# Performance work log

Hardware: AMD Instinct MI355X
Metric: run time of the kernel (lower is better)

The kernel has to match this reference:

```python
import jax, jax.numpy as jnp
import numpy as np


def _lin_relu(V, W, b):
    # LinearEmbedding: matmul + bias + ReLU (with_act_func=True default)
    return jax.nn.relu(jnp.matmul(V, W) + b)


def setup_inputs() -> dict:
    key = jax.random.key(0)
    ks = jax.random.split(key, 8)
    B, N, F = 4, 4096, 512
    C = F // 8
    sx = 1.0 / np.sqrt(F)
    return {
        "V": jax.random.normal(ks[0], (B, N, F), dtype=jnp.float32),
        "Wf": jax.random.normal(ks[1], (F, C), dtype=jnp.float32) * sx,
        "bf": jax.random.normal(ks[2], (C,), dtype=jnp.float32) * 5e-5 + 1e-4,
        "Wg": jax.random.normal(ks[3], (F, C), dtype=jnp.float32) * sx,
        "bg": jax.random.normal(ks[4], (C,), dtype=jnp.float32) * 5e-5 + 1e-4,
        "Wh": jax.random.normal(ks[5], (F, F), dtype=jnp.float32) * sx,
        "bh": jax.random.normal(ks[6], (F,), dtype=jnp.float32) * 5e-5 + 1e-4,
        "gamma": jax.random.normal(ks[7], (F,), dtype=jnp.float32),
    }


def reference(V, Wf, bf, Wg, bg, Wh, bh, gamma):
    f_out = _lin_relu(V, Wf, bf)          # [B, N, C]
    g_out = _lin_relu(V, Wg, bg)          # [B, N, C]
    h_out = _lin_relu(V, Wh, bh)          # [B, N, F]
    scores = jnp.einsum('bnc,bmc->bnm', f_out, g_out)  # [B, N, N]
    s = jax.nn.softmax(scores, axis=-1)
    o = jnp.einsum('bnm,bmf->bnf', s, h_out)            # [B, N, F]
    return gamma * o + V
```

## Files before the change

### kernel.cpp

```cpp
#include <hip/hip_runtime.h>
#include <hip/hip_bf16.h>
#include <math.h>

#define M_ROWS 16384
#define F_DIM 512
#define C_DIM 64

typedef short bf16x8 __attribute__((ext_vector_type(8)));
typedef float floatx4 __attribute__((ext_vector_type(4)));
typedef unsigned short ushortx8 __attribute__((ext_vector_type(8)));
typedef unsigned short ushortx4 __attribute__((ext_vector_type(4)));

static __device__ __forceinline__ unsigned short f2bf(float x) {
    __hip_bfloat16 h = __float2bfloat16(x);
    return *reinterpret_cast<unsigned short*>(&h);
}
static __device__ __forceinline__ float bf2f(unsigned short h) {
    unsigned int u = ((unsigned int)h) << 16;
    return __builtin_bit_cast(float, u);
}

static __device__ __forceinline__ void lgkm_barrier() {
    asm volatile("s_waitcnt lgkmcnt(0)\n\ts_barrier" ::: "memory");
}


__global__ __launch_bounds__(64) void prep_w_kernel(
    const float* __restrict__ Wf, const float* __restrict__ Wg,
    const float* __restrict__ Wh,
    unsigned short* __restrict__ wt_hi, unsigned short* __restrict__ wt_lo)
{
    const int c = blockIdx.x;
    const int t = threadIdx.x;
    const float* W; int ld, cl;
    if (c < 64)       { W = Wf; ld = C_DIM; cl = c; }
    else if (c < 128) { W = Wg; ld = C_DIM; cl = c - 64; }
    else              { W = Wh; ld = F_DIM; cl = c - 128; }
    const int ng = c >> 4, l16 = c & 15;
    for (int k = t; k < F_DIM; k += 64) {
        const float x = W[(size_t)k * ld + cl];
        const unsigned short h = f2bf(x);
        const int kh = k >> 5, qd = (k >> 3) & 3, j = k & 7;
        const size_t off = (((size_t)(ng * 16 + kh) * 64) + qd * 16 + l16) * 8 + j;
        wt_hi[off] = h;
        wt_lo[off] = f2bf(x - bf2f(h));
    }
}

#define BM 64
#define LDK 72

__global__ __launch_bounds__(256, 4) void embed_mfma_kernel(
    const float* __restrict__ V,
    const unsigned short* __restrict__ wt_hi, const unsigned short* __restrict__ wt_lo,
    const float* __restrict__ bf, const float* __restrict__ bg,
    const float* __restrict__ bh,
    unsigned short* __restrict__ f_bf, unsigned short* __restrict__ g_bf,
    unsigned short* __restrict__ h_sw)
{
    __shared__ __align__(16) unsigned short a_hi[BM][LDK];
    __shared__ __align__(16) unsigned short a_lo[BM][LDK];

    const int t  = threadIdx.x;
    const int R0 = blockIdx.x * BM;
    const bool fg = (blockIdx.y == 0);
    const int cbase = fg ? 0 : blockIdx.y * 128;

    const int w = t >> 6, lane = t & 63, quad = lane >> 4, l16 = lane & 15;

    floatx4 acc[4][2];
    #pragma unroll
    for (int rt = 0; rt < 4; ++rt)
        #pragma unroll
        for (int c = 0; c < 2; ++c)
            acc[rt][c] = (floatx4){0.f, 0.f, 0.f, 0.f};

    const int arow = t >> 4;
    const int acol = (t & 15) * 4;
    const int ng0  = (cbase >> 4) + w * 2;

    #pragma unroll 1
    for (int k0 = 0; k0 < F_DIM; k0 += 64) {
        lgkm_barrier();
        #pragma unroll
        for (int rr = 0; rr < 4; ++rr) {
            const int row = rr * 16 + arow;
            const float4 x = *(const float4*)(V + (size_t)(R0 + row) * F_DIM + k0 + acol);
            const float xs[4] = {x.x, x.y, x.z, x.w};
            ushortx4 hi, lo;
            #pragma unroll
            for (int jj = 0; jj < 4; ++jj) {
                const unsigned short hb2 = f2bf(xs[jj]);
                hi[jj] = hb2;
                lo[jj] = f2bf(xs[jj] - bf2f(hb2));
            }
            *(ushortx4*)&a_hi[row][acol] = hi;
            if (fg) *(ushortx4*)&a_lo[row][acol] = lo;
        }
        lgkm_barrier();
        #pragma unroll
        for (int kk = 0; kk < 2; ++kk) {
            const int kh = (k0 >> 5) + kk;
            const bf16x8 b0 = *(const bf16x8*)(wt_hi + (((size_t)(ng0 * 16 + kh)) * 64 + lane) * 8);
            const bf16x8 b1 = *(const bf16x8*)(wt_hi + (((size_t)((ng0 + 1) * 16 + kh)) * 64 + lane) * 8);
            bf16x8 ah[4];
            #pragma unroll
            for (int rt = 0; rt < 4; ++rt)
                ah[rt] = *(const bf16x8*)&a_hi[rt * 16 + l16][kk * 32 + quad * 8];
            #pragma unroll
            for (int rt = 0; rt < 4; ++rt) {
                acc[rt][0] = __builtin_amdgcn_mfma_f32_16x16x32_bf16(ah[rt], b0, acc[rt][0], 0, 0, 0);
                acc[rt][1] = __builtin_amdgcn_mfma_f32_16x16x32_bf16(ah[rt], b1, acc[rt][1], 0, 0, 0);
            }
            if (fg) {
                const bf16x8 c0 = *(const bf16x8*)(wt_lo + (((size_t)(ng0 * 16 + kh)) * 64 + lane) * 8);
                const bf16x8 c1 = *(const bf16x8*)(wt_lo + (((size_t)((ng0 + 1) * 16 + kh)) * 64 + lane) * 8);
                bf16x8 al[4];
                #pragma unroll
                for (int rt = 0; rt < 4; ++rt)
                    al[rt] = *(const bf16x8*)&a_lo[rt * 16 + l16][kk * 32 + quad * 8];
                #pragma unroll
                for (int rt = 0; rt < 4; ++rt) {
                    acc[rt][0] = __builtin_amdgcn_mfma_f32_16x16x32_bf16(ah[rt], c0, acc[rt][0], 0, 0, 0);
                    acc[rt][0] = __builtin_amdgcn_mfma_f32_16x16x32_bf16(al[rt], b0, acc[rt][0], 0, 0, 0);
                    acc[rt][1] = __builtin_amdgcn_mfma_f32_16x16x32_bf16(ah[rt], c1, acc[rt][1], 0, 0, 0);
                    acc[rt][1] = __builtin_amdgcn_mfma_f32_16x16x32_bf16(al[rt], b1, acc[rt][1], 0, 0, 0);
                }
            }
        }
    }

    #pragma unroll
    for (int rt = 0; rt < 4; ++rt) {
        #pragma unroll
        for (int c = 0; c < 2; ++c) {
            const int wtc  = cbase + w * 32 + c * 16 + l16;
            const int rowl = rt * 16 + quad * 4;
            const float bias = fg ? (wtc < 64 ? bf[wtc] : bg[wtc - 64]) : bh[wtc - 128];
            const floatx4 v = acc[rt][c];
            if (fg) {
                unsigned short* dst = (wtc < 64) ? (f_bf + wtc) : (g_bf + wtc - 64);
                #pragma unroll
                for (int r = 0; r < 4; ++r) {
                    const float z = v[r] + bias;
                    dst[(size_t)(R0 + rowl + r) * C_DIM] = f2bf(z > 0.f ? z : 0.f);
                }
            } else {
                const int hc   = wtc - 128;
                const int grow = R0 + rowl;
                const int b    = grow >> 12, rl = grow & 4095;
                const int T    = rl >> 6, mloc = rl & 63;
                const int kh2  = mloc >> 5, q2 = (mloc >> 3) & 3, j0 = mloc & 7;
                ushortx4 st;
                #pragma unroll
                for (int r = 0; r < 4; ++r) {
                    const float z = v[r] + bias;
                    st[r] = f2bf(z > 0.f ? z : 0.f);
                }
                const size_t off = ((((size_t)(b * 64 + T) * 64) + (hc >> 4) * 2 + kh2) * 64
                                    + q2 * 16 + (hc & 15)) * 8 + j0;
                *(ushortx4*)(h_sw + off) = st;
            }
        }
    }
}

#define QT 64
#define KT 64

__global__ __launch_bounds__(1024, 4) void attn_mfma_kernel(
    const unsigned short* __restrict__ f_bf, const unsigned short* __restrict__ g_bf,
    const unsigned short* __restrict__ h_sw, const float* __restrict__ gamma,
    const float* __restrict__ V, float* __restrict__ out)
{
    __shared__ __align__(16) unsigned short p_lds[2][QT * 64];
    __shared__ __align__(16) unsigned short g_lds[2][KT * 64];
    __shared__ float l_red[4][QT];
    __shared__ float l_inv[QT];

    const int t = threadIdx.x;
    const int w = t >> 6, lane = t & 63, quad = lane >> 4, l16 = lane & 15;
    const int wr = w & 3, wc = w >> 2;

    const int bid  = blockIdx.x;
    const int orig = (bid & 7) * 32 + (bid >> 3);
    const int b    = orig >> 6, qb = orig & 63;
    const int R0   = qb * QT;

    const unsigned short* fb    = f_bf + ((size_t)b * 4096 + R0) * C_DIM;
    const unsigned short* gb    = g_bf + (size_t)b * 4096 * C_DIM;
    const unsigned short* hbase = h_sw + (size_t)b * 64 * 32768;

    bf16x8 f0, f1;
    {
        const unsigned short* fr = fb + (size_t)(wr * 16 + l16) * C_DIM + quad * 8;
        f0 = *(const bf16x8*)fr;
        f1 = *(const bf16x8*)(fr + 32);
    }
    const float gam0 = gamma[w * 32 + l16];
    const float gam1 = gamma[w * 32 + 16 + l16];

    floatx4 acc[4][2];
    #pragma unroll
    for (int rt = 0; rt < 4; ++rt)
        #pragma unroll
        for (int c = 0; c < 2; ++c)
            acc[rt][c] = (floatx4){0.f, 0.f, 0.f, 0.f};
    float run_l[4] = {0.f, 0.f, 0.f, 0.f};

    const int grow    = t >> 4, gk = (t & 15) * 4;
    const int g_swoff = grow * 128 + ((gk * 2) ^ ((grow & 7) << 4));
    ushortx4 greg = *(const ushortx4*)(gb + (size_t)grow * C_DIM + gk);

    const int sgrow   = wc * 16 + l16;
    const int sg_off0 = sgrow * 128 + ((quad * 16)      ^ ((sgrow & 7) << 4));
    const int sg_off1 = sgrow * 128 + ((quad * 16 + 64) ^ ((sgrow & 7) << 4));

    for (int it = 0; it < 64; ++it) {
        const int buf = it & 1;
        const unsigned short* ht = hbase + (size_t)it * 32768 + (size_t)(4 * w) * 512;

        const bf16x8 h0 = *(const bf16x8*)(ht + (size_t)lane * 8);
        const bf16x8 h1 = *(const bf16x8*)(ht + 512 + (size_t)lane * 8);
        const bf16x8 h2 = *(const bf16x8*)(ht + 1024 + (size_t)lane * 8);
        const bf16x8 h3 = *(const bf16x8*)(ht + 1536 + (size_t)lane * 8);

        *(ushortx4*)((unsigned char*)&g_lds[buf][0] + g_swoff) = greg;
        if (it < 63)
            greg = *(const ushortx4*)(gb + (size_t)((it + 1) * KT + grow) * C_DIM + gk);
        lgkm_barrier();

        const unsigned char* gB = (const unsigned char*)&g_lds[buf][0];
        unsigned char*       pB = (unsigned char*)&p_lds[buf][0];

        {
            const bf16x8 g0 = *(const bf16x8*)(gB + sg_off0);
            const bf16x8 g1 = *(const bf16x8*)(gB + sg_off1);
            floatx4 cc = (floatx4){0.f, 0.f, 0.f, 0.f};
            cc = __builtin_amdgcn_mfma_f32_16x16x32_bf16(f0, g0, cc, 0, 0, 0);
            cc = __builtin_amdgcn_mfma_f32_16x16x32_bf16(f1, g1, cc, 0, 0, 0);
            #pragma unroll
            for (int r = 0; r < 4; ++r) {
                const float p = __expf(cc[r] - 32.f);
                run_l[r] += p;
                const int prow = wr * 16 + quad * 4 + r;
                const int pcol = wc * 16 + l16;
                *(unsigned short*)(pB + prow * 128 + ((pcol * 2) ^ ((prow & 7) << 4))) = f2bf(p);
            }
        }
        lgkm_barrier();

        #pragma unroll
        for (int rt = 0; rt < 4; ++rt) {
            const int prow = rt * 16 + l16;
            const int sw   = (prow & 7) << 4;
            const bf16x8 pf0 = *(const bf16x8*)(pB + prow * 128 + ((quad * 16)      ^ sw));
            const bf16x8 pf1 = *(const bf16x8*)(pB + prow * 128 + ((quad * 16 + 64) ^ sw));
            acc[rt][0] = __builtin_amdgcn_mfma_f32_16x16x32_bf16(pf0, h0, acc[rt][0], 0, 0, 0);
            acc[rt][0] = __builtin_amdgcn_mfma_f32_16x16x32_bf16(pf1, h1, acc[rt][0], 0, 0, 0);
            acc[rt][1] = __builtin_amdgcn_mfma_f32_16x16x32_bf16(pf0, h2, acc[rt][1], 0, 0, 0);
            acc[rt][1] = __builtin_amdgcn_mfma_f32_16x16x32_bf16(pf1, h3, acc[rt][1], 0, 0, 0);
        }
    }

    #pragma unroll
    for (int r = 0; r < 4; ++r) {
        float v = run_l[r];
        v += __shfl_xor(v, 1, 64);
        v += __shfl_xor(v, 2, 64);
        v += __shfl_xor(v, 4, 64);
        v += __shfl_xor(v, 8, 64);
        if (l16 == 0) l_red[wc][wr * 16 + quad * 4 + r] = v;
    }
    __syncthreads();
    if (t < QT)
        l_inv[t] = 1.f / (l_red[0][t] + l_red[1][t] + l_red[2][t] + l_red[3][t]);
    __syncthreads();

    const float* Vb = V   + ((size_t)b * 4096 + R0) * F_DIM;
    float*       ob = out + ((size_t)b * 4096 + R0) * F_DIM;
    const int c0 = w * 32 + l16;
    #pragma unroll
    for (int rt = 0; rt < 4; ++rt) {
        #pragma unroll
        for (int r = 0; r < 4; ++r) {
            const int row = rt * 16 + quad * 4 + r;
            const float li = l_inv[row];
            ob[(size_t)row * F_DIM + c0]      = gam0 * acc[rt][0][r] * li + Vb[(size_t)row * F_DIM + c0];
            ob[(size_t)row * F_DIM + c0 + 16] = gam1 * acc[rt][1][r] * li + Vb[(size_t)row * F_DIM + c0 + 16];
        }
    }
}

extern "C" void kernel_launch(void* const* d_in, const int* in_sizes, int n_in,
                              void* d_out, int out_size, void* d_ws, size_t ws_size,
                              hipStream_t stream) {
    const float* V     = (const float*)d_in[0];
    const float* Wf    = (const float*)d_in[1];
    const float* bf    = (const float*)d_in[2];
    const float* Wg    = (const float*)d_in[3];
    const float* bg    = (const float*)d_in[4];
    const float* Wh    = (const float*)d_in[5];
    const float* bh    = (const float*)d_in[6];
    const float* gamma = (const float*)d_in[7];
    float* out = (float*)d_out;

    unsigned short* f_bf  = (unsigned short*)d_ws;
    unsigned short* g_bf  = f_bf + (size_t)M_ROWS * C_DIM;
    unsigned short* h_sw  = g_bf + (size_t)M_ROWS * C_DIM;
    unsigned short* wt_hi = h_sw + (size_t)4 * F_DIM * 4096;
    unsigned short* wt_lo = wt_hi + (size_t)640 * F_DIM;

    prep_w_kernel<<<640, 64, 0, stream>>>(Wf, Wg, Wh, wt_hi, wt_lo);
    embed_mfma_kernel<<<dim3(M_ROWS / BM, 5), 256, 0, stream>>>(
        V, wt_hi, wt_lo, bf, bg, bh, f_bf, g_bf, h_sw);
    attn_mfma_kernel<<<256, 1024, 0, stream>>>(f_bf, g_bf, h_sw, gamma, V, out);
}
```

Baseline: 203.5 us.

## Halve attention query tile and widen per-wave output columns

The attention kernel now processes 32 query rows per block with 512 threads instead of 64 rows with 1024 threads, launching 512 blocks. Each wave now owns 64 output feature columns (four accumulator groups) and loads eight H fragments per key tile. The G tile load is widened to 8-element vectors. The aim is smaller blocks with lighter barrier coupling and more MFMA work per wave. The cost is that every H tile is re-read by twice as many blocks, and each wave holds more registers for H fragments.

```diff
diff --git a/kernel.cpp b/kernel.cpp
--- a/kernel.cpp
+++ b/kernel.cpp
@@ -165,10 +165,10 @@
     }
 }
 
-#define QT 64
+#define QT 32
 #define KT 64
 
-__global__ __launch_bounds__(1024, 4) void attn_mfma_kernel(
+__global__ __launch_bounds__(512, 4) void attn_mfma_kernel(
     const unsigned short* __restrict__ f_bf, const unsigned short* __restrict__ g_bf,
     const unsigned short* __restrict__ h_sw, const float* __restrict__ gamma,
     const float* __restrict__ V, float* __restrict__ out)
@@ -180,11 +180,11 @@
 
     const int t = threadIdx.x;
     const int w = t >> 6, lane = t & 63, quad = lane >> 4, l16 = lane & 15;
-    const int wr = w & 3, wc = w >> 2;
+    const int wr = w & 1, wc = w >> 1;
 
     const int bid  = blockIdx.x;
-    const int orig = (bid & 7) * 32 + (bid >> 3);
-    const int b    = orig >> 6, qb = orig & 63;
+    const int orig = (bid & 7) * 64 + (bid >> 3);
+    const int b    = orig >> 7, qb = orig & 127;
     const int R0   = qb * QT;
 
     const unsigned short* fb    = f_bf + ((size_t)b * 4096 + R0) * C_DIM;
@@ -197,20 +197,22 @@
         f0 = *(const bf16x8*)fr;
         f1 = *(const bf16x8*)(fr + 32);
     }
-    const float gam0 = gamma[w * 32 + l16];
-    const float gam1 = gamma[w * 32 + 16 + l16];
-
-    floatx4 acc[4][2];
-    #pragma unroll
-    for (int rt = 0; rt < 4; ++rt)
-        #pragma unroll
-        for (int c = 0; c < 2; ++c)
-            acc[rt][c] = (floatx4){0.f, 0.f, 0.f, 0.f};
+    float gam[4];
+    #pragma unroll
+    for (int cg = 0; cg < 4; ++cg)
+        gam[cg] = gamma[w * 64 + cg * 16 + l16];
+
+    floatx4 acc[2][4];
+    #pragma unroll
+    for (int rt = 0; rt < 2; ++rt)
+        #pragma unroll
+        for (int cg = 0; cg < 4; ++cg)
+            acc[rt][cg] = (floatx4){0.f, 0.f, 0.f, 0.f};
     float run_l[4] = {0.f, 0.f, 0.f, 0.f};
 
-    const int grow    = t >> 4, gk = (t & 15) * 4;
-    const int g_swoff = grow * 128 + ((gk * 2) ^ ((grow & 7) << 4));
-    ushortx4 greg = *(const ushortx4*)(gb + (size_t)grow * C_DIM + gk);
+    const int grow    = t >> 3, gck = (t & 7) * 16;
+    const int g_swoff = grow * 128 + (gck ^ ((grow & 7) << 4));
+    ushortx8 greg = *(const ushortx8*)(gb + (size_t)grow * C_DIM + (t & 7) * 8);
 
     const int sgrow   = wc * 16 + l16;
     const int sg_off0 = sgrow * 128 + ((quad * 16)      ^ ((sgrow & 7) << 4));
@@ -218,16 +220,16 @@
 
     for (int it = 0; it < 64; ++it) {
         const int buf = it & 1;
-        const unsigned short* ht = hbase + (size_t)it * 32768 + (size_t)(4 * w) * 512;
-
-        const bf16x8 h0 = *(const bf16x8*)(ht + (size_t)lane * 8);
-        const bf16x8 h1 = *(const bf16x8*)(ht + 512 + (size_t)lane * 8);
-        const bf16x8 h2 = *(const bf16x8*)(ht + 1024 + (size_t)lane * 8);
-        const bf16x8 h3 = *(const bf16x8*)(ht + 1536 + (size_t)lane * 8);
-
-        *(ushortx4*)((unsigned char*)&g_lds[buf][0] + g_swoff) = greg;
+        const unsigned short* ht = hbase + (size_t)it * 32768 + (size_t)w * 4096;
+
+        bf16x8 h[8];
+        #pragma unroll
+        for (int gi = 0; gi < 8; ++gi)
+            h[gi] = *(const bf16x8*)(ht + gi * 512 + (size_t)lane * 8);
+
+        *(ushortx8*)((unsigned char*)&g_lds[buf][0] + g_swoff) = greg;
         if (it < 63)
-            greg = *(const ushortx4*)(gb + (size_t)((it + 1) * KT + grow) * C_DIM + gk);
+            greg = *(const ushortx8*)(gb + (size_t)((it + 1) * KT + grow) * C_DIM + (t & 7) * 8);
         lgkm_barrier();
 
         const unsigned char* gB = (const unsigned char*)&g_lds[buf][0];
@@ -251,15 +253,16 @@
         lgkm_barrier();
 
         #pragma unroll
-        for (int rt = 0; rt < 4; ++rt) {
+        for (int rt = 0; rt < 2; ++rt) {
             const int prow = rt * 16 + l16;
             const int sw   = (prow & 7) << 4;
             const bf16x8 pf0 = *(const bf16x8*)(pB + prow * 128 + ((quad * 16)      ^ sw));
             const bf16x8 pf1 = *(const bf16x8*)(pB + prow * 128 + ((quad * 16 + 64) ^ sw));
-            acc[rt][0] = __builtin_amdgcn_mfma_f32_16x16x32_bf16(pf0, h0, acc[rt][0], 0, 0, 0);
-            acc[rt][0] = __builtin_amdgcn_mfma_f32_16x16x32_bf16(pf1, h1, acc[rt][0], 0, 0, 0);
-            acc[rt][1] = __builtin_amdgcn_mfma_f32_16x16x32_bf16(pf0, h2, acc[rt][1], 0, 0, 0);
-            acc[rt][1] = __builtin_amdgcn_mfma_f32_16x16x32_bf16(pf1, h3, acc[rt][1], 0, 0, 0);
+            #pragma unroll
+            for (int cg = 0; cg < 4; ++cg) {
+                acc[rt][cg] = __builtin_amdgcn_mfma_f32_16x16x32_bf16(pf0, h[2 * cg],     acc[rt][cg], 0, 0, 0);
+                acc[rt][cg] = __builtin_amdgcn_mfma_f32_16x16x32_bf16(pf1, h[2 * cg + 1], acc[rt][cg], 0, 0, 0);
+            }
         }
     }
 
@@ -279,15 +282,18 @@
 
     const float* Vb = V   + ((size_t)b * 4096 + R0) * F_DIM;
     float*       ob = out + ((size_t)b * 4096 + R0) * F_DIM;
-    const int c0 = w * 32 + l16;
-    #pragma unroll
-    for (int rt = 0; rt < 4; ++rt) {
+    #pragma unroll
+    for (int rt = 0; rt < 2; ++rt) {
         #pragma unroll
         for (int r = 0; r < 4; ++r) {
             const int row = rt * 16 + quad * 4 + r;
             const float li = l_inv[row];
-            ob[(size_t)row * F_DIM + c0]      = gam0 * acc[rt][0][r] * li + Vb[(size_t)row * F_DIM + c0];
-            ob[(size_t)row * F_DIM + c0 + 16] = gam1 * acc[rt][1][r] * li + Vb[(size_t)row * F_DIM + c0 + 16];
+            #pragma unroll
+            for (int cg = 0; cg < 4; ++cg) {
+                const int col = w * 64 + cg * 16 + l16;
+                ob[(size_t)row * F_DIM + col] =
+                    gam[cg] * acc[rt][cg][r] * li + Vb[(size_t)row * F_DIM + col];
+            }
         }
     }
 }
@@ -314,5 +320,5 @@
     prep_w_kernel<<<640, 64, 0, stream>>>(Wf, Wg, Wh, wt_hi, wt_lo);
     embed_mfma_kernel<<<dim3(M_ROWS / BM, 5), 256, 0, stream>>>(
         V, wt_hi, wt_lo, bf, bg, bh, f_bf, g_bf, h_sw);
-    attn_mfma_kernel<<<256, 1024, 0, stream>>>(f_bf, g_bf, h_sw, gamma, V, out);
-}
+    attn_mfma_kernel<<<512, 512, 0, stream>>>(f_bf, g_bf, h_sw, gamma, V, out);
+}
```

Result: slower. 222.3 us (+9.3%).

## Retile attention blocks to 128 query rows by half the feature columns

Applied to the files above, without the earlier changes.

Each block now covers 128 query rows and 256 of the 512 output features. Two blocks split the feature dimension, with the block index mapping batch, column half and query tile. Each wave loads half as many h fragments per key tile and computes a 16x32 score tile. The aim is to halve per-block h bandwidth relative to the output rows, at the cost of computing QK^T and softmax twice, once in each column-half block.

```diff
diff --git a/kernel.cpp b/kernel.cpp
--- a/kernel.cpp
+++ b/kernel.cpp
@@ -165,7 +165,7 @@
     }
 }
 
-#define QT 64
+#define QT 128
 #define KT 64
 
 __global__ __launch_bounds__(1024, 4) void attn_mfma_kernel(
@@ -175,55 +175,55 @@
 {
     __shared__ __align__(16) unsigned short p_lds[2][QT * 64];
     __shared__ __align__(16) unsigned short g_lds[2][KT * 64];
-    __shared__ float l_red[4][QT];
+    __shared__ float l_red[2][QT];
     __shared__ float l_inv[QT];
 
     const int t = threadIdx.x;
     const int w = t >> 6, lane = t & 63, quad = lane >> 4, l16 = lane & 15;
-    const int wr = w & 3, wc = w >> 2;
-
-    const int bid  = blockIdx.x;
-    const int orig = (bid & 7) * 32 + (bid >> 3);
-    const int b    = orig >> 6, qb = orig & 63;
-    const int R0   = qb * QT;
+    const int sr = (w & 7) * 16, sc = (w >> 3) * 32;
+
+    const int bid = blockIdx.x;
+    const int b   = (bid & 7) >> 1;
+    const int ch  = bid & 1;
+    const int qb  = bid >> 3;
+    const int R0  = qb * QT;
 
     const unsigned short* fb    = f_bf + ((size_t)b * 4096 + R0) * C_DIM;
     const unsigned short* gb    = g_bf + (size_t)b * 4096 * C_DIM;
     const unsigned short* hbase = h_sw + (size_t)b * 64 * 32768;
+    const int hgrp = (ch * 16 + w) * 2;
 
     bf16x8 f0, f1;
     {
-        const unsigned short* fr = fb + (size_t)(wr * 16 + l16) * C_DIM + quad * 8;
+        const unsigned short* fr = fb + (size_t)(sr + l16) * C_DIM + quad * 8;
         f0 = *(const bf16x8*)fr;
         f1 = *(const bf16x8*)(fr + 32);
     }
-    const float gam0 = gamma[w * 32 + l16];
-    const float gam1 = gamma[w * 32 + 16 + l16];
-
-    floatx4 acc[4][2];
-    #pragma unroll
-    for (int rt = 0; rt < 4; ++rt)
-        #pragma unroll
-        for (int c = 0; c < 2; ++c)
-            acc[rt][c] = (floatx4){0.f, 0.f, 0.f, 0.f};
+    const float gam = gamma[ch * 256 + w * 16 + l16];
+
+    floatx4 acc[8];
+    #pragma unroll
+    for (int rt = 0; rt < 8; ++rt)
+        acc[rt] = (floatx4){0.f, 0.f, 0.f, 0.f};
     float run_l[4] = {0.f, 0.f, 0.f, 0.f};
 
     const int grow    = t >> 4, gk = (t & 15) * 4;
     const int g_swoff = grow * 128 + ((gk * 2) ^ ((grow & 7) << 4));
     ushortx4 greg = *(const ushortx4*)(gb + (size_t)grow * C_DIM + gk);
 
-    const int sgrow   = wc * 16 + l16;
-    const int sg_off0 = sgrow * 128 + ((quad * 16)      ^ ((sgrow & 7) << 4));
-    const int sg_off1 = sgrow * 128 + ((quad * 16 + 64) ^ ((sgrow & 7) << 4));
+    const int sgrow0  = sc + l16;
+    const int sgrow1  = sc + 16 + l16;
+    const int sg0_off0 = sgrow0 * 128 + ((quad * 16)      ^ ((sgrow0 & 7) << 4));
+    const int sg0_off1 = sgrow0 * 128 + ((quad * 16 + 64) ^ ((sgrow0 & 7) << 4));
+    const int sg1_off0 = sgrow1 * 128 + ((quad * 16)      ^ ((sgrow1 & 7) << 4));
+    const int sg1_off1 = sgrow1 * 128 + ((quad * 16 + 64) ^ ((sgrow1 & 7) << 4));
 
     for (int it = 0; it < 64; ++it) {
         const int buf = it & 1;
-        const unsigned short* ht = hbase + (size_t)it * 32768 + (size_t)(4 * w) * 512;
+        const unsigned short* ht = hbase + (size_t)it * 32768 + (size_t)hgrp * 512;
 
         const bf16x8 h0 = *(const bf16x8*)(ht + (size_t)lane * 8);
         const bf16x8 h1 = *(const bf16x8*)(ht + 512 + (size_t)lane * 8);
-        const bf16x8 h2 = *(const bf16x8*)(ht + 1024 + (size_t)lane * 8);
-        const bf16x8 h3 = *(const bf16x8*)(ht + 1536 + (size_t)lane * 8);
 
         *(ushortx4*)((unsigned char*)&g_lds[buf][0] + g_swoff) = greg;
         if (it < 63)
@@ -234,32 +234,37 @@
         unsigned char*       pB = (unsigned char*)&p_lds[buf][0];
 
         {
-            const bf16x8 g0 = *(const bf16x8*)(gB + sg_off0);
-            const bf16x8 g1 = *(const bf16x8*)(gB + sg_off1);
+            const bf16x8 ga0 = *(const bf16x8*)(gB + sg0_off0);
+            const bf16x8 ga1 = *(const bf16x8*)(gB + sg0_off1);
             floatx4 cc = (floatx4){0.f, 0.f, 0.f, 0.f};
-            cc = __builtin_amdgcn_mfma_f32_16x16x32_bf16(f0, g0, cc, 0, 0, 0);
-            cc = __builtin_amdgcn_mfma_f32_16x16x32_bf16(f1, g1, cc, 0, 0, 0);
+            cc = __builtin_amdgcn_mfma_f32_16x16x32_bf16(f0, ga0, cc, 0, 0, 0);
+            cc = __builtin_amdgcn_mfma_f32_16x16x32_bf16(f1, ga1, cc, 0, 0, 0);
+            const bf16x8 gb0 = *(const bf16x8*)(gB + sg1_off0);
+            const bf16x8 gb1 = *(const bf16x8*)(gB + sg1_off1);
+            floatx4 cd = (floatx4){0.f, 0.f, 0.f, 0.f};
+            cd = __builtin_amdgcn_mfma_f32_16x16x32_bf16(f0, gb0, cd, 0, 0, 0);
+            cd = __builtin_amdgcn_mfma_f32_16x16x32_bf16(f1, gb1, cd, 0, 0, 0);
             #pragma unroll
             for (int r = 0; r < 4; ++r) {
-                const float p = __expf(cc[r] - 32.f);
-                run_l[r] += p;
-                const int prow = wr * 16 + quad * 4 + r;
-                const int pcol = wc * 16 + l16;
-                *(unsigned short*)(pB + prow * 128 + ((pcol * 2) ^ ((prow & 7) << 4))) = f2bf(p);
+                const int prow = sr + quad * 4 + r;
+                const int swp  = (prow & 7) << 4;
+                const float p0 = __expf(cc[r] - 32.f);
+                const float p1 = __expf(cd[r] - 32.f);
+                run_l[r] += p0 + p1;
+                *(unsigned short*)(pB + prow * 128 + (((sc + l16) * 2)      ^ swp)) = f2bf(p0);
+                *(unsigned short*)(pB + prow * 128 + (((sc + 16 + l16) * 2) ^ swp)) = f2bf(p1);
             }
         }
         lgkm_barrier();
 
         #pragma unroll
-        for (int rt = 0; rt < 4; ++rt) {
+        for (int rt = 0; rt < 8; ++rt) {
             const int prow = rt * 16 + l16;
             const int sw   = (prow & 7) << 4;
             const bf16x8 pf0 = *(const bf16x8*)(pB + prow * 128 + ((quad * 16)      ^ sw));
             const bf16x8 pf1 = *(const bf16x8*)(pB + prow * 128 + ((quad * 16 + 64) ^ sw));
-            acc[rt][0] = __builtin_amdgcn_mfma_f32_16x16x32_bf16(pf0, h0, acc[rt][0], 0, 0, 0);
-            acc[rt][0] = __builtin_amdgcn_mfma_f32_16x16x32_bf16(pf1, h1, acc[rt][0], 0, 0, 0);
-            acc[rt][1] = __builtin_amdgcn_mfma_f32_16x16x32_bf16(pf0, h2, acc[rt][1], 0, 0, 0);
-            acc[rt][1] = __builtin_amdgcn_mfma_f32_16x16x32_bf16(pf1, h3, acc[rt][1], 0, 0, 0);
+            acc[rt] = __builtin_amdgcn_mfma_f32_16x16x32_bf16(pf0, h0, acc[rt], 0, 0, 0);
+            acc[rt] = __builtin_amdgcn_mfma_f32_16x16x32_bf16(pf1, h1, acc[rt], 0, 0, 0);
         }
     }
 
@@ -270,24 +275,23 @@
         v += __shfl_xor(v, 2, 64);
         v += __shfl_xor(v, 4, 64);
         v += __shfl_xor(v, 8, 64);
-        if (l16 == 0) l_red[wc][wr * 16 + quad * 4 + r] = v;
+        if (l16 == 0) l_red[w >> 3][sr + quad * 4 + r] = v;
     }
     __syncthreads();
     if (t < QT)
-        l_inv[t] = 1.f / (l_red[0][t] + l_red[1][t] + l_red[2][t] + l_red[3][t]);
+        l_inv[t] = 1.f / (l_red[0][t] + l_red[1][t]);
     __syncthreads();
 
     const float* Vb = V   + ((size_t)b * 4096 + R0) * F_DIM;
     float*       ob = out + ((size_t)b * 4096 + R0) * F_DIM;
-    const int c0 = w * 32 + l16;
-    #pragma unroll
-    for (int rt = 0; rt < 4; ++rt) {
+    const int col = ch * 256 + w * 16 + l16;
+    #pragma unroll
+    for (int rt = 0; rt < 8; ++rt) {
         #pragma unroll
         for (int r = 0; r < 4; ++r) {
             const int row = rt * 16 + quad * 4 + r;
-            const float li = l_inv[row];
-            ob[(size_t)row * F_DIM + c0]      = gam0 * acc[rt][0][r] * li + Vb[(size_t)row * F_DIM + c0];
-            ob[(size_t)row * F_DIM + c0 + 16] = gam1 * acc[rt][1][r] * li + Vb[(size_t)row * F_DIM + c0 + 16];
+            ob[(size_t)row * F_DIM + col] =
+                gam * acc[rt][r] * l_inv[row] + Vb[(size_t)row * F_DIM + col];
         }
     }
 }
```

Measured after the change: 217.3 us. 6.8% more time.

## Software-pipeline attention loop: compute scores one step ahead of PV, 128-key steps

Applied to the files above, without the earlier changes.

Restructures the attention main loop so each iteration handles 128 keys as two 64-key sub-tiles. It computes the QK scores and exponentials for the next step while the PV MFMAs consume the previous step's P tile from a double buffer, which removes one barrier per iteration. It also widens the G loads to 8-element vectors and raises wave priority around the PV MFMA block. The cost is more LDS and more registers for the two sets of H fragments, which may hurt occupancy at 1024 threads.

```diff
diff --git a/kernel.cpp b/kernel.cpp
--- a/kernel.cpp
+++ b/kernel.cpp
@@ -166,15 +166,14 @@
 }
 
 #define QT 64
-#define KT 64
 
 __global__ __launch_bounds__(1024, 4) void attn_mfma_kernel(
     const unsigned short* __restrict__ f_bf, const unsigned short* __restrict__ g_bf,
     const unsigned short* __restrict__ h_sw, const float* __restrict__ gamma,
     const float* __restrict__ V, float* __restrict__ out)
 {
-    __shared__ __align__(16) unsigned short p_lds[2][QT * 64];
-    __shared__ __align__(16) unsigned short g_lds[2][KT * 64];
+    __shared__ __align__(16) unsigned short p_lds[2][2][QT * 64];
+    __shared__ __align__(16) unsigned short g_lds[2][2][64 * 64];
     __shared__ float l_red[4][QT];
     __shared__ float l_inv[QT];
 
@@ -208,32 +207,59 @@
             acc[rt][c] = (floatx4){0.f, 0.f, 0.f, 0.f};
     float run_l[4] = {0.f, 0.f, 0.f, 0.f};
 
-    const int grow    = t >> 4, gk = (t & 15) * 4;
-    const int g_swoff = grow * 128 + ((gk * 2) ^ ((grow & 7) << 4));
-    ushortx4 greg = *(const ushortx4*)(gb + (size_t)grow * C_DIM + gk);
+    const int grow = t >> 3, gchunk = t & 7;
+    const int ghalf = grow >> 6, gr64 = grow & 63;
+    const int g_swoff = gr64 * 128 + ((gchunk * 16) ^ ((gr64 & 7) << 4));
+    ushortx8 greg = *(const ushortx8*)(gb + (size_t)grow * C_DIM + gchunk * 8);
 
     const int sgrow   = wc * 16 + l16;
     const int sg_off0 = sgrow * 128 + ((quad * 16)      ^ ((sgrow & 7) << 4));
     const int sg_off1 = sgrow * 128 + ((quad * 16 + 64) ^ ((sgrow & 7) << 4));
 
-    for (int it = 0; it < 64; ++it) {
-        const int buf = it & 1;
-        const unsigned short* ht = hbase + (size_t)it * 32768 + (size_t)(4 * w) * 512;
-
-        const bf16x8 h0 = *(const bf16x8*)(ht + (size_t)lane * 8);
-        const bf16x8 h1 = *(const bf16x8*)(ht + 512 + (size_t)lane * 8);
-        const bf16x8 h2 = *(const bf16x8*)(ht + 1024 + (size_t)lane * 8);
-        const bf16x8 h3 = *(const bf16x8*)(ht + 1536 + (size_t)lane * 8);
-
-        *(ushortx4*)((unsigned char*)&g_lds[buf][0] + g_swoff) = greg;
-        if (it < 63)
-            greg = *(const ushortx4*)(gb + (size_t)((it + 1) * KT + grow) * C_DIM + gk);
+    *(ushortx8*)((unsigned char*)&g_lds[0][ghalf][0] + g_swoff) = greg;
+    greg = *(const ushortx8*)(gb + (size_t)(128 + grow) * C_DIM + gchunk * 8);
+    lgkm_barrier();
+    #pragma unroll
+    for (int s = 0; s < 2; ++s) {
+        const unsigned char* gB = (const unsigned char*)&g_lds[0][s][0];
+        unsigned char*       pB = (unsigned char*)&p_lds[0][s][0];
+        const bf16x8 g0 = *(const bf16x8*)(gB + sg_off0);
+        const bf16x8 g1 = *(const bf16x8*)(gB + sg_off1);
+        floatx4 cc = (floatx4){0.f, 0.f, 0.f, 0.f};
+        cc = __builtin_amdgcn_mfma_f32_16x16x32_bf16(f0, g0, cc, 0, 0, 0);
+        cc = __builtin_amdgcn_mfma_f32_16x16x32_bf16(f1, g1, cc, 0, 0, 0);
+        #pragma unroll
+        for (int r = 0; r < 4; ++r) {
+            const float p = __expf(cc[r] - 32.f);
+            run_l[r] += p;
+            const int prow = wr * 16 + quad * 4 + r;
+            const int pcol = wc * 16 + l16;
+            *(unsigned short*)(pB + prow * 128 + ((pcol * 2) ^ ((prow & 7) << 4))) = f2bf(p);
+        }
+    }
+
+    bf16x8 h[2][4];
+
+    for (int it = 1; it < 32; ++it) {
+        const int buf = it & 1, pb = buf ^ 1;
+
+        const unsigned short* ht0 = hbase + (size_t)(2 * (it - 1)) * 32768 + (size_t)(4 * w) * 512;
+        const unsigned short* ht1 = ht0 + 32768;
+        #pragma unroll
+        for (int gi = 0; gi < 4; ++gi) {
+            h[0][gi] = *(const bf16x8*)(ht0 + gi * 512 + (size_t)lane * 8);
+            h[1][gi] = *(const bf16x8*)(ht1 + gi * 512 + (size_t)lane * 8);
+        }
+
+        *(ushortx8*)((unsigned char*)&g_lds[buf][ghalf][0] + g_swoff) = greg;
+        if (it < 31)
+            greg = *(const ushortx8*)(gb + (size_t)((it + 1) * 128 + grow) * C_DIM + gchunk * 8);
         lgkm_barrier();
 
-        const unsigned char* gB = (const unsigned char*)&g_lds[buf][0];
-        unsigned char*       pB = (unsigned char*)&p_lds[buf][0];
-
-        {
+        #pragma unroll
+        for (int s = 0; s < 2; ++s) {
+            const unsigned char* gB = (const unsigned char*)&g_lds[buf][s][0];
+            unsigned char*       pB = (unsigned char*)&p_lds[buf][s][0];
             const bf16x8 g0 = *(const bf16x8*)(gB + sg_off0);
             const bf16x8 g1 = *(const bf16x8*)(gB + sg_off1);
             floatx4 cc = (floatx4){0.f, 0.f, 0.f, 0.f};
@@ -248,18 +274,49 @@
                 *(unsigned short*)(pB + prow * 128 + ((pcol * 2) ^ ((prow & 7) << 4))) = f2bf(p);
             }
         }
-        lgkm_barrier();
-
+
+        __builtin_amdgcn_s_setprio(1);
         #pragma unroll
         for (int rt = 0; rt < 4; ++rt) {
             const int prow = rt * 16 + l16;
             const int sw   = (prow & 7) << 4;
-            const bf16x8 pf0 = *(const bf16x8*)(pB + prow * 128 + ((quad * 16)      ^ sw));
-            const bf16x8 pf1 = *(const bf16x8*)(pB + prow * 128 + ((quad * 16 + 64) ^ sw));
-            acc[rt][0] = __builtin_amdgcn_mfma_f32_16x16x32_bf16(pf0, h0, acc[rt][0], 0, 0, 0);
-            acc[rt][0] = __builtin_amdgcn_mfma_f32_16x16x32_bf16(pf1, h1, acc[rt][0], 0, 0, 0);
-            acc[rt][1] = __builtin_amdgcn_mfma_f32_16x16x32_bf16(pf0, h2, acc[rt][1], 0, 0, 0);
-            acc[rt][1] = __builtin_amdgcn_mfma_f32_16x16x32_bf16(pf1, h3, acc[rt][1], 0, 0, 0);
+            #pragma unroll
+            for (int s = 0; s < 2; ++s) {
+                const unsigned char* pB = (const unsigned char*)&p_lds[pb][s][0];
+                const bf16x8 pf0 = *(const bf16x8*)(pB + prow * 128 + ((quad * 16)      ^ sw));
+                const bf16x8 pf1 = *(const bf16x8*)(pB + prow * 128 + ((quad * 16 + 64) ^ sw));
+                acc[rt][0] = __builtin_amdgcn_mfma_f32_16x16x32_bf16(pf0, h[s][0], acc[rt][0], 0, 0, 0);
+                acc[rt][0] = __builtin_amdgcn_mfma_f32_16x16x32_bf16(pf1, h[s][1], acc[rt][0], 0, 0, 0);
+                acc[rt][1] = __builtin_amdgcn_mfma_f32_16x16x32_bf16(pf0, h[s][2], acc[rt][1], 0, 0, 0);
+                acc[rt][1] = __builtin_amdgcn_mfma_f32_16x16x32_bf16(pf1, h[s][3], acc[rt][1], 0, 0, 0);
+            }
+        }
+        __builtin_amdgcn_s_setprio(0);
+    }
+
+    {
+        const unsigned short* ht0 = hbase + (size_t)62 * 32768 + (size_t)(4 * w) * 512;
+        const unsigned short* ht1 = ht0 + 32768;
+        #pragma unroll
+        for (int gi = 0; gi < 4; ++gi) {
+            h[0][gi] = *(const bf16x8*)(ht0 + gi * 512 + (size_t)lane * 8);
+            h[1][gi] = *(const bf16x8*)(ht1 + gi * 512 + (size_t)lane * 8);
+        }
+        lgkm_barrier();
+        #pragma unroll
+        for (int rt = 0; rt < 4; ++rt) {
+            const int prow = rt * 16 + l16;
+            const int sw   = (prow & 7) << 4;
+            #pragma unroll
+            for (int s = 0; s < 2; ++s) {
+                const unsigned char* pB = (const unsigned char*)&p_lds[1][s][0];
+                const bf16x8 pf0 = *(const bf16x8*)(pB + prow * 128 + ((quad * 16)      ^ sw));
+                const bf16x8 pf1 = *(const bf16x8*)(pB + prow * 128 + ((quad * 16 + 64) ^ sw));
+                acc[rt][0] = __builtin_amdgcn_mfma_f32_16x16x32_bf16(pf0, h[s][0], acc[rt][0], 0, 0, 0);
+                acc[rt][0] = __builtin_amdgcn_mfma_f32_16x16x32_bf16(pf1, h[s][1], acc[rt][0], 0, 0, 0);
+                acc[rt][1] = __builtin_amdgcn_mfma_f32_16x16x32_bf16(pf0, h[s][2], acc[rt][1], 0, 0, 0);
+                acc[rt][1] = __builtin_amdgcn_mfma_f32_16x16x32_bf16(pf1, h[s][3], acc[rt][1], 0, 0, 0);
+            }
         }
     }
 
@@ -279,13 +336,13 @@
 
     const float* Vb = V   + ((size_t)b * 4096 + R0) * F_DIM;
     float*       ob = out + ((size_t)b * 4096 + R0) * F_DIM;
-    const int c0 = w * 32 + l16;
     #pragma unroll
     for (int rt = 0; rt < 4; ++rt) {
         #pragma unroll
         for (int r = 0; r < 4; ++r) {
             const int row = rt * 16 + quad * 4 + r;
             const float li = l_inv[row];
+            const int c0 = w * 32 + l16;
             ob[(size_t)row * F_DIM + c0]      = gam0 * acc[rt][0][r] * li + Vb[(size_t)row * F_DIM + c0];
             ob[(size_t)row * F_DIM + c0 + 16] = gam1 * acc[rt][1][r] * li + Vb[(size_t)row * F_DIM + c0 + 16];
         }
```

After: 204.4 us. Within noise of the previous version (+0.5%).
